# Optimization experiments

Hardware: AMD Instinct MI355X
Metric: run time of the kernel (lower is better)

## Reference

```python
import jax, jax.numpy as jnp
import numpy as np

UNITS = 512
CONN = 512          # input feature dim (connections)
DEND_SIZE = 16
SEQL = CONN // DEND_SIZE  # 32 dendrite segments per unit
BATCH = 512


def _make_dendrites(units, conn, dsize, seed=0):
    # Per-unit random permutation of input indices, grouped into contiguous
    # dendrites of size dsize -> segment id in [0, seql) for every input index.
    rng = np.random.default_rng(seed)
    seql = conn // dsize
    seg = np.empty((units, conn), dtype=np.int32)
    for u in range(units):
        perm = rng.permutation(conn)
        for s in range(seql):
            seg[u, perm[dsize * s:dsize * (s + 1)]] = s
    return seg


def setup_inputs() -> dict:
    key = jax.random.key(0)
    k1, k2, k3, k4 = jax.random.split(key, 4)
    x = jax.random.normal(k1, (BATCH, CONN), dtype=jnp.float32)
    # weight_twice & not uniqueW -> per-unit scalar input weight, shape [1, units]
    kernel = jax.random.uniform(k2, (1, UNITS), dtype=jnp.float32, minval=5e-5, maxval=0.1)
    # per-(segment, unit) dendritic weight, shape [seql, units]
    dendriticW = jax.random.uniform(k3, (SEQL, UNITS), dtype=jnp.float32, minval=5e-5, maxval=0.1)
    bias = jax.random.normal(k4, (UNITS,), dtype=jnp.float32) * 0.05
    dendrites = jnp.asarray(_make_dendrites(UNITS, CONN, DEND_SIZE))  # [units, conn] int32
    return {"x": x, "kernel": kernel, "dendriticW": dendriticW,
            "bias": bias, "dendrites": dendrites}


def reference(x, kernel, dendriticW, bias, dendrites):
    # x: [batch, conn]; dendrites: [units, conn] segment ids in [0, SEQL)
    xT = x.T  # [conn, batch]
    # per-unit gather + unsorted_segment_sum over connections -> [units, seql, batch]
    segsum = jax.vmap(lambda seg: jax.ops.segment_sum(xT, seg, num_segments=SEQL))(dendrites)
    # weight_twice: per-unit scalar input weight (kernel broadcast over conn)
    segsum = segsum * kernel[0][:, None, None]
    # dendritic weighting + reduction over segments -> [batch, units]
    out = jnp.einsum('usb,su->bu', segsum, dendriticW) + bias
    return jax.nn.relu(out)
```

## Files before the change

### kernel.cpp

```cpp
#include <hip/hip_runtime.h>
#include <hip/hip_bf16.h>

#define UNITS 512
#define CONN  512
#define SEQL  32

typedef __hip_bfloat16 bf16;
typedef __attribute__((ext_vector_type(8))) short short8;
typedef __attribute__((ext_vector_type(4))) float floatx4;


union cv8 { bf16 h[8]; short8 v; };

__global__ __launch_bounds__(256) void prep(
    const float* __restrict__ kern,
    const float* __restrict__ dW,
    const int*   __restrict__ dend,
    const float* __restrict__ x,
    bf16* __restrict__ W,
    bf16* __restrict__ xb,
    int nxthreads)
{
    __shared__ float table[4][SEQL];
    const int tid = blockIdx.x * 256 + threadIdx.x;
    const int WTHREADS = UNITS * (CONN / 8);

    if (tid < WTHREADS) {
        const int u    = tid >> 6;
        const int lane = threadIdx.x & 63;
        const int wid  = threadIdx.x >> 6;
        if (lane < SEQL)
            table[wid][lane] = dW[lane * UNITS + u];
        __syncthreads();

        const int c0 = lane * 8;
        const float kv = kern[u];
        const int4 s0 = ((const int4*)(dend + u * CONN + c0))[0];
        const int4 s1 = ((const int4*)(dend + u * CONN + c0))[1];
        const int segs[8] = {s0.x, s0.y, s0.z, s0.w, s1.x, s1.y, s1.z, s1.w};
        cv8 w;
#pragma unroll
        for (int i = 0; i < 8; ++i)
            w.h[i] = __float2bfloat16(kv * table[wid][segs[i]]);
        *(short8*)(W + u * CONN + c0) = w.v;
    } else {
        __syncthreads();
        const int t = tid - WTHREADS;
        if (t < nxthreads) {
            const float4 f0 = ((const float4*)x)[t * 2];
            const float4 f1 = ((const float4*)x)[t * 2 + 1];
            cv8 a;
            a.h[0] = __float2bfloat16(f0.x); a.h[1] = __float2bfloat16(f0.y);
            a.h[2] = __float2bfloat16(f0.z); a.h[3] = __float2bfloat16(f0.w);
            a.h[4] = __float2bfloat16(f1.x); a.h[5] = __float2bfloat16(f1.y);
            a.h[6] = __float2bfloat16(f1.z); a.h[7] = __float2bfloat16(f1.w);
            *(short8*)(xb + t * 8) = a.v;
        }
    }
}

__global__ __launch_bounds__(64) void gemm_mfma(
    const bf16*  __restrict__ xb,
    const bf16*  __restrict__ W,
    const float* __restrict__ bias,
    float* __restrict__ out)
{
    const int lane = threadIdx.x;
    const int ut = blockIdx.x * 16;
    const int bt = blockIdx.y * 16;
    const int m = lane & 15;
    const int q = lane >> 4;

    const bf16* xrow = xb + (size_t)(bt + m) * CONN + q * 8;
    const bf16* wrow = W  + (size_t)(ut + m) * CONN + q * 8;

    floatx4 acc = {0.f, 0.f, 0.f, 0.f};
#pragma unroll
    for (int k = 0; k < CONN; k += 32) {
        const short8 a = *(const short8*)(xrow + k);
        const short8 b = *(const short8*)(wrow + k);
        acc = __builtin_amdgcn_mfma_f32_16x16x32_bf16(a, b, acc, 0, 0, 0);
    }

    const float bu = bias[ut + m];
#pragma unroll
    for (int r = 0; r < 4; ++r) {
        float v = acc[r] + bu;
        v = v > 0.f ? v : 0.f;
        out[(size_t)(bt + q * 4 + r) * UNITS + ut + m] = v;
    }
}

__device__ __forceinline__ short8 cvt8(const float* p) {
    const float4 f0 = ((const float4*)p)[0];
    const float4 f1 = ((const float4*)p)[1];
    cv8 a;
    a.h[0] = __float2bfloat16(f0.x); a.h[1] = __float2bfloat16(f0.y);
    a.h[2] = __float2bfloat16(f0.z); a.h[3] = __float2bfloat16(f0.w);
    a.h[4] = __float2bfloat16(f1.x); a.h[5] = __float2bfloat16(f1.y);
    a.h[6] = __float2bfloat16(f1.z); a.h[7] = __float2bfloat16(f1.w);
    return a.v;
}

__global__ __launch_bounds__(256) void dendriter_fused_mfma(
    const float* __restrict__ x, const float* __restrict__ kern,
    const float* __restrict__ dW, const float* __restrict__ bias,
    const int* __restrict__ dend, float* __restrict__ out)
{
    __shared__ short8 wl[16][65];
    const int t  = threadIdx.x;
    const int ut = blockIdx.x * 16;
    const int bt = blockIdx.y * 64;
    {
        const int ul  = t >> 4;
        const int cg0 = (t & 15) * 4;
        const int u   = ut + ul;
        const float kv = kern[u];
        const int4* dp = (const int4*)(dend + u * CONN + cg0 * 8);
#pragma unroll
        for (int j = 0; j < 4; ++j) {
            const int4 s0 = dp[2 * j];
            const int4 s1 = dp[2 * j + 1];
            const int segs[8] = {s0.x, s0.y, s0.z, s0.w, s1.x, s1.y, s1.z, s1.w};
            cv8 w;
#pragma unroll
            for (int i = 0; i < 8; ++i)
                w.h[i] = __float2bfloat16(kv * dW[segs[i] * UNITS + u]);
            const int cg = cg0 + j;
            wl[cg >> 2][ul | ((cg & 3) << 4)] = w.v;
        }
    }
    __syncthreads();

    const int lane = t & 63;
    const int wv   = t >> 6;
    const int m = lane & 15;
    const int q = lane >> 4;
    const int btw = bt + wv * 16;
    const float* xrow = x + (size_t)(btw + m) * CONN + q * 8;
    floatx4 acc = {0.f, 0.f, 0.f, 0.f};
#pragma unroll
    for (int kb = 0; kb < 16; ++kb) {
        const short8 a = cvt8(xrow + kb * 32);
        const short8 b = wl[kb][lane];
        acc = __builtin_amdgcn_mfma_f32_16x16x32_bf16(a, b, acc, 0, 0, 0);
    }
    const float bu = bias[ut + m];
#pragma unroll
    for (int r = 0; r < 4; ++r) {
        float v = acc[r] + bu;
        v = v > 0.f ? v : 0.f;
        out[(size_t)(btw + q * 4 + r) * UNITS + ut + m] = v;
    }
}

extern "C" void kernel_launch(void* const* d_in, const int* in_sizes, int n_in,
                              void* d_out, int out_size, void* d_ws, size_t ws_size,
                              hipStream_t stream) {
    const float* x    = (const float*)d_in[0];
    const float* kern = (const float*)d_in[1];
    const float* dW   = (const float*)d_in[2];
    const float* bias = (const float*)d_in[3];
    const int*   dend = (const int*)  d_in[4];
    float* out = (float*)d_out;

    const int batch = in_sizes[0] / CONN;
    const size_t w_bytes  = (size_t)UNITS * CONN * sizeof(bf16);
    const size_t xb_bytes = (size_t)batch * CONN * sizeof(bf16);
    const int nxthreads = batch * CONN / 8;

    if (ws_size >= w_bytes + xb_bytes) {
        bf16* W  = (bf16*)d_ws;
        bf16* xb = W + (size_t)UNITS * CONN;
        prep<<<(UNITS * CONN / 8 + nxthreads + 255) / 256, 256, 0, stream>>>(
            kern, dW, dend, x, W, xb, nxthreads);
        gemm_mfma<<<dim3(UNITS / 16, batch / 16), 64, 0, stream>>>(xb, W, bias, out);
    } else {
        dendriter_fused_mfma<<<dim3(UNITS / 16, batch / 64), 256, 0, stream>>>(
            x, kern, dW, bias, dend, out);
    }
}
```

Measured before the change: 66.63 us.

## Merge prep and GEMM into one cooperative kernel with grid sync

Replaces the two-kernel sequence (prep conversion, then MFMA GEMM) with a single cooperative launch of 256 blocks. The first 128 blocks build the bf16 weight matrix and the rest convert x to bf16, then a grid-wide sync separates this from the GEMM phase, where each wave computes one 16x16 output tile. The aim is to remove the second kernel launch and its inter-kernel gap. In exchange it adds a grid barrier and a cooperative-launch requirement, and the path is restricted to batch == 512.

Result: slower. 143.0 us (+114.5%).

```diff
diff --git a/kernel.cpp b/kernel.cpp
--- a/kernel.cpp
+++ b/kernel.cpp
@@ -1,9 +1,12 @@
 #include <hip/hip_runtime.h>
 #include <hip/hip_bf16.h>
+#include <hip/hip_cooperative_groups.h>
 
 #define UNITS 512
 #define CONN  512
 #define SEQL  32
+
+namespace cg = cooperative_groups;
 
 typedef __hip_bfloat16 bf16;
 typedef __attribute__((ext_vector_type(8))) short short8;
@@ -12,23 +15,24 @@
 
 union cv8 { bf16 h[8]; short8 v; };
 
-__global__ __launch_bounds__(256) void prep(
+__global__ __launch_bounds__(256) void dendriter_coop(
+    const float* __restrict__ x,
     const float* __restrict__ kern,
     const float* __restrict__ dW,
+    const float* __restrict__ bias,
     const int*   __restrict__ dend,
-    const float* __restrict__ x,
     bf16* __restrict__ W,
     bf16* __restrict__ xb,
-    int nxthreads)
+    float* __restrict__ out)
 {
     __shared__ float table[4][SEQL];
-    const int tid = blockIdx.x * 256 + threadIdx.x;
-    const int WTHREADS = UNITS * (CONN / 8);
+    const int b = blockIdx.x;
+    const int t = threadIdx.x;
+    const int wid  = t >> 6;
+    const int lane = t & 63;
 
-    if (tid < WTHREADS) {
-        const int u    = tid >> 6;
-        const int lane = threadIdx.x & 63;
-        const int wid  = threadIdx.x >> 6;
+    if (b < 128) {
+        const int u = b * 4 + wid;
         if (lane < SEQL)
             table[wid][lane] = dW[lane * UNITS + u];
         __syncthreads();
@@ -44,30 +48,23 @@
             w.h[i] = __float2bfloat16(kv * table[wid][segs[i]]);
         *(short8*)(W + u * CONN + c0) = w.v;
     } else {
-        __syncthreads();
-        const int t = tid - WTHREADS;
-        if (t < nxthreads) {
-            const float4 f0 = ((const float4*)x)[t * 2];
-            const float4 f1 = ((const float4*)x)[t * 2 + 1];
-            cv8 a;
-            a.h[0] = __float2bfloat16(f0.x); a.h[1] = __float2bfloat16(f0.y);
-            a.h[2] = __float2bfloat16(f0.z); a.h[3] = __float2bfloat16(f0.w);
-            a.h[4] = __float2bfloat16(f1.x); a.h[5] = __float2bfloat16(f1.y);
-            a.h[6] = __float2bfloat16(f1.z); a.h[7] = __float2bfloat16(f1.w);
-            *(short8*)(xb + t * 8) = a.v;
-        }
+        const int t2 = (b - 128) * 256 + t;
+        const float4 f0 = ((const float4*)x)[t2 * 2];
+        const float4 f1 = ((const float4*)x)[t2 * 2 + 1];
+        cv8 a;
+        a.h[0] = __float2bfloat16(f0.x); a.h[1] = __float2bfloat16(f0.y);
+        a.h[2] = __float2bfloat16(f0.z); a.h[3] = __float2bfloat16(f0.w);
+        a.h[4] = __float2bfloat16(f1.x); a.h[5] = __float2bfloat16(f1.y);
+        a.h[6] = __float2bfloat16(f1.z); a.h[7] = __float2bfloat16(f1.w);
+        *(short8*)(xb + t2 * 8) = a.v;
     }
-}
 
-__global__ __launch_bounds__(64) void gemm_mfma(
-    const bf16*  __restrict__ xb,
-    const bf16*  __restrict__ W,
-    const float* __restrict__ bias,
-    float* __restrict__ out)
-{
-    const int lane = threadIdx.x;
-    const int ut = blockIdx.x * 16;
-    const int bt = blockIdx.y * 16;
+    __threadfence();
+    cg::this_grid().sync();
+
+    const int tile = b * 4 + wid;
+    const int ut = (tile & 31) * 16;
+    const int bt = (tile >> 5) * 16;
     const int m = lane & 15;
     const int q = lane >> 4;
 
@@ -78,8 +75,8 @@
 #pragma unroll
     for (int k = 0; k < CONN; k += 32) {
         const short8 a = *(const short8*)(xrow + k);
-        const short8 b = *(const short8*)(wrow + k);
-        acc = __builtin_amdgcn_mfma_f32_16x16x32_bf16(a, b, acc, 0, 0, 0);
+        const short8 bb = *(const short8*)(wrow + k);
+        acc = __builtin_amdgcn_mfma_f32_16x16x32_bf16(a, bb, acc, 0, 0, 0);
     }
 
     const float bu = bias[ut + m];
@@ -142,8 +139,8 @@
 #pragma unroll
     for (int kb = 0; kb < 16; ++kb) {
         const short8 a = cvt8(xrow + kb * 32);
-        const short8 b = wl[kb][lane];
-        acc = __builtin_amdgcn_mfma_f32_16x16x32_bf16(a, b, acc, 0, 0, 0);
+        const short8 bfr = wl[kb][lane];
+        acc = __builtin_amdgcn_mfma_f32_16x16x32_bf16(a, bfr, acc, 0, 0, 0);
     }
     const float bu = bias[ut + m];
 #pragma unroll
@@ -167,14 +164,14 @@
     const int batch = in_sizes[0] / CONN;
     const size_t w_bytes  = (size_t)UNITS * CONN * sizeof(bf16);
     const size_t xb_bytes = (size_t)batch * CONN * sizeof(bf16);
-    const int nxthreads = batch * CONN / 8;
 
-    if (ws_size >= w_bytes + xb_bytes) {
+    if (ws_size >= w_bytes + xb_bytes && batch == 512) {
         bf16* W  = (bf16*)d_ws;
         bf16* xb = W + (size_t)UNITS * CONN;
-        prep<<<(UNITS * CONN / 8 + nxthreads + 255) / 256, 256, 0, stream>>>(
-            kern, dW, dend, x, W, xb, nxthreads);
-        gemm_mfma<<<dim3(UNITS / 16, batch / 16), 64, 0, stream>>>(xb, W, bias, out);
+        void* args[] = {(void*)&x, (void*)&kern, (void*)&dW, (void*)&bias,
+                        (void*)&dend, (void*)&W, (void*)&xb, (void*)&out};
+        hipLaunchCooperativeKernel((const void*)dendriter_coop,
+                                   dim3(256), dim3(256), args, 0, stream);
     } else {
         dendriter_fused_mfma<<<dim3(UNITS / 16, batch / 64), 256, 0, stream>>>(
             x, kern, dW, bias, dend, out);
```
